# Kernel optimization log

Hardware: AMD Instinct MI355X
Metric: run time of the kernel (lower is better)

## Reference

```python
import jax, jax.numpy as jnp
import numpy as np

B, T, C = 4, 2048, 2048
H, N = 32, 64  # heads, head_size
EPS = 1e-5


def setup_inputs() -> dict:
    key = jax.random.key(0)
    ks = jax.random.split(key, 16)
    s = 0.02
    return {
        'hidden': jax.random.normal(ks[0], (B, T, C), jnp.float32),
        'time_decay': jax.random.normal(ks[1], (H, N), jnp.float32),
        'time_first': jax.random.normal(ks[2], (H, N), jnp.float32),
        'Wr': jax.random.normal(ks[3], (C, C), jnp.float32) * s,
        'Wk': jax.random.normal(ks[4], (C, C), jnp.float32) * s,
        'Wv': jax.random.normal(ks[5], (C, C), jnp.float32) * s,
        'Wg': jax.random.normal(ks[6], (C, C), jnp.float32) * s,
        'Wo': jax.random.normal(ks[7], (C, C), jnp.float32) * s,
        'mix_r': jax.random.uniform(ks[8], (1, 1, C), jnp.float32),
        'mix_k': jax.random.uniform(ks[9], (1, 1, C), jnp.float32),
        'mix_v': jax.random.uniform(ks[10], (1, 1, C), jnp.float32),
        'mix_g': jax.random.uniform(ks[11], (1, 1, C), jnp.float32),
        'ln_w': jax.random.uniform(ks[12], (C,), jnp.float32, 0.5, 1.5),
        'ln_b': jax.random.normal(ks[13], (C,), jnp.float32) * 0.1,
        'init_state': jnp.zeros((B, H, N, N), jnp.float32),
    }


def reference(hidden, time_decay, time_first, Wr, Wk, Wv, Wg, Wo,
              mix_r, mix_k, mix_v, mix_g, ln_w, ln_b, init_state):
    b, t, c = hidden.shape
    h, n = time_decay.shape
    # time shift: shifted[:, 0] = 0 (fresh state), shifted[:, i] = hidden[:, i-1]
    shifted = jnp.pad(hidden, ((0, 0), (1, 0), (0, 0)))[:, :-1]
    xk = hidden * mix_k + shifted * (1.0 - mix_k)
    xv = hidden * mix_v + shifted * (1.0 - mix_v)
    xr = hidden * mix_r + shifted * (1.0 - mix_r)
    xg = hidden * mix_g + shifted * (1.0 - mix_g)

    r = (xr @ Wr).astype(jnp.float32).reshape(b, t, h, n)
    k = (xk @ Wk).astype(jnp.float32).reshape(b, t, h, n)
    v = (xv @ Wv).astype(jnp.float32).reshape(b, t, h, n)
    gate = jax.nn.silu(xg @ Wg)  # [b,t,c]

    w = jnp.exp(-jnp.exp(time_decay.astype(jnp.float32)))  # [h,n] decay per k-channel
    u = time_first.astype(jnp.float32)                      # [h,n]

    def step(state, rkv):
        rt, kt, vt = rkv  # each [b,h,n]
        at = kt[..., :, None] * vt[..., None, :]  # outer product kt @ vt -> [b,h,n,n]
        out_t = jnp.einsum('bhn,bhnm->bhm', rt, u[None, :, :, None] * at + state)
        new_state = at + w[None, :, :, None] * state
        return new_state, out_t

    rT = jnp.moveaxis(r, 1, 0)  # [t,b,h,n]
    kT = jnp.moveaxis(k, 1, 0)
    vT = jnp.moveaxis(v, 1, 0)
    final_state, outT = jax.lax.scan(step, init_state.astype(jnp.float32), (rT, kT, vT))
    out = jnp.moveaxis(outT, 0, 1)  # [b,t,h,n]

    # GroupNorm with num_groups = h over the c = h*n channels
    mean = out.mean(-1, keepdims=True)
    var = out.var(-1, keepdims=True)
    out = (out - mean) / jnp.sqrt(var + EPS)
    out = out.reshape(b, t, c) * ln_w + ln_b

    out = out.astype(hidden.dtype) * gate
    out = out @ Wo
    return out, final_state
```

## Files before the change

### kernel.cpp

```cpp
#include <hip/hip_runtime.h>
#include <stdint.h>

typedef unsigned short ushort_t;
typedef __attribute__((ext_vector_type(8))) short bf16x8;
typedef __attribute__((ext_vector_type(4))) float f32x4;
typedef __attribute__((ext_vector_type(8))) unsigned short u16x8;

__device__ __forceinline__ ushort_t f2bf(float f) {
  union { float f; unsigned u; } v; v.f = f;
  unsigned r = v.u + 0x7fffu + ((v.u >> 16) & 1u);
  return (ushort_t)(r >> 16);
}
__device__ __forceinline__ float bf2f(ushort_t u) {
  union { unsigned u; float f; } v; v.u = ((unsigned)u) << 16;
  return v.f;
}

__device__ __forceinline__ void gload_lds16(const void* g, void* l) {
  __builtin_amdgcn_global_load_lds(
      (const __attribute__((address_space(1))) void*)g,
      (__attribute__((address_space(3))) void*)l, 16, 0, 0);
}

struct PrepArgs {
  const float* W[5];
  ushort_t* Wt[5];
  const float* Hd;
  const float* mr; const float* mk; const float* mv; const float* mg;
  ushort_t* xr; ushort_t* xk; ushort_t* xv; ushort_t* xg;
};

__global__ __launch_bounds__(256) void prep(PrepArgs a, int n, int Mrows, int Tt) {
  const int z = blockIdx.z;
  if (z < 5) {
    const float* __restrict__ W = a.W[z];
    ushort_t* __restrict__ Wt = a.Wt[z];
    __shared__ float tile[32][33];
    const int tx = threadIdx.x & 31, ty = threadIdx.x >> 5;
    const int bx = blockIdx.x, by = blockIdx.y;
#pragma unroll
    for (int r = 0; r < 4; ++r)
      tile[ty + 8 * r][tx] = W[(size_t)(by * 32 + ty + 8 * r) * n + bx * 32 + tx];
    __syncthreads();
#pragma unroll
    for (int r = 0; r < 4; ++r)
      Wt[(size_t)(bx * 32 + ty + 8 * r) * n + by * 32 + tx] =
          f2bf(tile[tx][ty + 8 * r]);
    return;
  }
  const int Cc = n;
  const float* __restrict__ Hd = a.Hd;
  const size_t n8 = (size_t)Mrows * Cc / 8;
  const int bid = blockIdx.y * gridDim.x + blockIdx.x;
  for (size_t idx = (size_t)bid * blockDim.x + threadIdx.x; idx < n8;
       idx += (size_t)gridDim.x * gridDim.y * blockDim.x) {
    const size_t e = idx * 8;
    const int m = (int)(e / (size_t)Cc);
    const int c = (int)(e % (size_t)Cc);
    const int t = m % Tt;
    f32x4 h0 = *(const f32x4*)&Hd[e];
    f32x4 h1 = *(const f32x4*)&Hd[e + 4];
    f32x4 sA = {0.f, 0.f, 0.f, 0.f}, sB = {0.f, 0.f, 0.f, 0.f};
    if (t != 0) {
      sA = *(const f32x4*)&Hd[e - Cc];
      sB = *(const f32x4*)&Hd[e - Cc + 4];
    }
    f32x4 mA[4], mB[4];
    mA[0] = *(const f32x4*)&a.mr[c]; mB[0] = *(const f32x4*)&a.mr[c + 4];
    mA[1] = *(const f32x4*)&a.mk[c]; mB[1] = *(const f32x4*)&a.mk[c + 4];
    mA[2] = *(const f32x4*)&a.mv[c]; mB[2] = *(const f32x4*)&a.mv[c + 4];
    mA[3] = *(const f32x4*)&a.mg[c]; mB[3] = *(const f32x4*)&a.mg[c + 4];
    u16x8 o[4];
#pragma unroll
    for (int w = 0; w < 4; ++w) {
#pragma unroll
      for (int q = 0; q < 4; ++q) {
        o[w][q]     = f2bf(sA[q] + (h0[q] - sA[q]) * mA[w][q]);
        o[w][q + 4] = f2bf(sB[q] + (h1[q] - sB[q]) * mB[w][q]);
      }
    }
    *(u16x8*)&a.xr[e] = o[0];
    *(u16x8*)&a.xk[e] = o[1];
    *(u16x8*)&a.xv[e] = o[2];
    *(u16x8*)&a.xg[e] = o[3];
  }
}

struct GemmArgs {
  const ushort_t* A[4];
  const ushort_t* Bt[4];
  void* C[4];
};

__device__ __forceinline__ void stage_mat(const ushort_t* __restrict__ base,
                                          int K, int voff, char* ldsmat,
                                          int tid) {
#pragma unroll
  for (int hf = 0; hf < 2; ++hf)
#pragma unroll
    for (int s = 0; s < 2; ++s)
      gload_lds16(base + (size_t)(hf * 128 + s * 64) * K + voff,
                  ldsmat + hf * 16384 + s * 8192 + tid * 16);
}

template <int BF16OUT>
__global__ __launch_bounds__(512, 1) void gemm256(GemmArgs args, int M, int N, int K) {
  extern __shared__ char lds[];
  const int z = blockIdx.z;
  const ushort_t* __restrict__ A = args.A[z];
  const ushort_t* __restrict__ Bt = args.Bt[z];

  const int tid = threadIdx.x;
  const int lane = tid & 63, w = tid >> 6;
  const int wm = w >> 2, wn = w & 3;
  const int r16 = lane & 15, kb = lane >> 4;

  const int nbx = N >> 8;
  const int nwg = nbx * (M >> 8);
  const int orig = blockIdx.y * nbx + blockIdx.x;
  const int wid = (orig & 7) * (nwg >> 3) + (orig >> 3);
  const int bm0 = (wid / nbx) << 8;
  const int bn0 = (wid % nbx) << 8;

  const int trow = tid >> 3;
  const int voff = trow * K + (((((tid & 7) * 16) ^ ((trow & 7) << 4))) >> 1);
  const ushort_t* __restrict__ Abase = A + (size_t)bm0 * K;
  const ushort_t* __restrict__ Bbase = Bt + (size_t)bn0 * K;

  int aoff[8], boff[4];
#pragma unroll
  for (int mi = 0; mi < 8; ++mi) {
    const int d = (mi * 16 + r16) * 128 + kb * 16;
    aoff[mi] = wm * 16384 + (d ^ (((d >> 7) & 7) << 4));
  }
#pragma unroll
  for (int ni = 0; ni < 4; ++ni) {
    const int d = ((wn & 1) * 64 + ni * 16 + r16) * 128 + kb * 16;
    boff[ni] = 32768 + (wn >> 1) * 16384 + (d ^ (((d >> 7) & 7) << 4));
  }

  f32x4 acc[8][4] = {};
  const int NT = K >> 6;

  stage_mat(Abase, K, voff, lds, tid);
  stage_mat(Bbase, K, voff, lds + 32768, tid);
  stage_mat(Abase + 64, K, voff, lds + 65536, tid);
  stage_mat(Bbase + 64, K, voff, lds + 65536 + 32768, tid);
  asm volatile("s_waitcnt vmcnt(8)" ::: "memory");
  asm volatile("s_barrier" ::: "memory");

  for (int t = 0; t < NT; ++t) {
    const int cur = t & 1;
    char* cbase = lds + cur * 65536;
    bf16x8 ah[4][2], bq[4][2];

#pragma unroll
    for (int m = 0; m < 4; ++m) {
      ah[m][0] = *(const bf16x8*)(cbase + aoff[m]);
      ah[m][1] = *(const bf16x8*)(cbase + (aoff[m] ^ 64));
    }
#pragma unroll
    for (int n = 0; n < 2; ++n) {
      bq[n][0] = *(const bf16x8*)(cbase + boff[n]);
      bq[n][1] = *(const bf16x8*)(cbase + (boff[n] ^ 64));
    }
    asm volatile("s_barrier" ::: "memory");
    __builtin_amdgcn_s_setprio(1);
#pragma unroll
    for (int m = 0; m < 4; ++m)
#pragma unroll
      for (int n = 0; n < 2; ++n)
#pragma unroll
        for (int ks = 0; ks < 2; ++ks)
          acc[m][n] = __builtin_amdgcn_mfma_f32_16x16x32_bf16(
              ah[m][ks], bq[n][ks], acc[m][n], 0, 0, 0);
    __builtin_amdgcn_s_setprio(0);

#pragma unroll
    for (int n = 2; n < 4; ++n) {
      bq[n][0] = *(const bf16x8*)(cbase + boff[n]);
      bq[n][1] = *(const bf16x8*)(cbase + (boff[n] ^ 64));
    }
    asm volatile("s_barrier" ::: "memory");
    __builtin_amdgcn_s_setprio(1);
#pragma unroll
    for (int m = 0; m < 4; ++m)
#pragma unroll
      for (int n = 2; n < 4; ++n)
#pragma unroll
        for (int ks = 0; ks < 2; ++ks)
          acc[m][n] = __builtin_amdgcn_mfma_f32_16x16x32_bf16(
              ah[m][ks], bq[n][ks], acc[m][n], 0, 0, 0);
    __builtin_amdgcn_s_setprio(0);

#pragma unroll
    for (int m = 0; m < 4; ++m) {
      ah[m][0] = *(const bf16x8*)(cbase + aoff[4 + m]);
      ah[m][1] = *(const bf16x8*)(cbase + (aoff[4 + m] ^ 64));
    }
    asm volatile("s_barrier" ::: "memory");
    if (t + 2 < NT)
      stage_mat(Abase + (t + 2) * 64, K, voff, cbase, tid);
    __builtin_amdgcn_s_setprio(1);
#pragma unroll
    for (int m = 0; m < 4; ++m)
#pragma unroll
      for (int n = 0; n < 2; ++n)
#pragma unroll
        for (int ks = 0; ks < 2; ++ks)
          acc[4 + m][n] = __builtin_amdgcn_mfma_f32_16x16x32_bf16(
              ah[m][ks], bq[n][ks], acc[4 + m][n], 0, 0, 0);

    if (t + 2 < NT)
      stage_mat(Bbase + (t + 2) * 64, K, voff, cbase + 32768, tid);
#pragma unroll
    for (int m = 0; m < 4; ++m)
#pragma unroll
      for (int n = 2; n < 4; ++n)
#pragma unroll
        for (int ks = 0; ks < 2; ++ks)
          acc[4 + m][n] = __builtin_amdgcn_mfma_f32_16x16x32_bf16(
              ah[m][ks], bq[n][ks], acc[4 + m][n], 0, 0, 0);
    __builtin_amdgcn_s_setprio(0);

    if (t + 1 < NT) {
      if (t + 2 < NT)
        asm volatile("s_waitcnt vmcnt(8)" ::: "memory");
      else
        asm volatile("s_waitcnt vmcnt(0)" ::: "memory");
      asm volatile("s_barrier" ::: "memory");
    }
  }

  const int row0 = bm0 + wm * 128 + kb * 4;
  const int col0 = bn0 + wn * 64 + r16;
#pragma unroll
  for (int mi = 0; mi < 8; ++mi)
#pragma unroll
    for (int ni = 0; ni < 4; ++ni) {
      f32x4 v = acc[mi][ni];
      const int row = row0 + mi * 16;
      const int col = col0 + ni * 16;
#pragma unroll
      for (int rr = 0; rr < 4; ++rr) {
        if (BF16OUT)
          ((ushort_t*)args.C[z])[(size_t)(row + rr) * N + col] = f2bf(v[rr]);
        else
          ((float*)args.C[z])[(size_t)(row + rr) * N + col] = v[rr];
      }
    }
}

__global__ __launch_bounds__(512, 1) void wkv_chunk(
    const ushort_t* __restrict__ Rm, const ushort_t* __restrict__ Km,
    const ushort_t* __restrict__ Vm, const float* __restrict__ td,
    const float* __restrict__ tf,
    float* __restrict__ Oatt, float* __restrict__ chunkA,
    int Tt, int Hh, int NC, int Lc) {
  extern __shared__ char smem[];
  ushort_t* Rs = (ushort_t*)(smem + 0);
  ushort_t* Ks = (ushort_t*)(smem + 18432);
  ushort_t* Vt = (ushort_t*)(smem + 36864);
  ushort_t* Kt = (ushort_t*)(smem + 54272);
  ushort_t* At = (ushort_t*)(smem + 71680);
  float* wp  = (float*)(smem + 106496);
  float* u_  = (float*)(smem + 110848);
  float* l2w = (float*)(smem + 111104);

  const int blk = blockIdx.x;
  const int bh = blk / NC, c = blk % NC;
  const int b = bh / Hh, h = bh % Hh;
  const int tid = threadIdx.x;
  const int lane = tid & 63, w = tid >> 6;
  const int r16 = lane & 15, g = lane >> 4;
  const int Cc = Hh * 64;
  const size_t base = ((size_t)b * Tt + (size_t)c * Lc) * Cc + h * 64;

  {
    const int srow = tid >> 2;
    const int scol = (tid & 3) * 16;
    const size_t gb = base + (size_t)srow * Cc + scol;
    u16x8 r0 = *(const u16x8*)&Rm[gb];
    u16x8 r1 = *(const u16x8*)&Rm[gb + 8];
    u16x8 k0 = *(const u16x8*)&Km[gb];
    u16x8 k1 = *(const u16x8*)&Km[gb + 8];
    u16x8 v0 = *(const u16x8*)&Vm[gb];
    u16x8 v1 = *(const u16x8*)&Vm[gb + 8];
    *(u16x8*)&Rs[srow * 72 + scol] = r0;
    *(u16x8*)&Rs[srow * 72 + scol + 8] = r1;
    *(u16x8*)&Ks[srow * 72 + scol] = k0;
    *(u16x8*)&Ks[srow * 72 + scol + 8] = k1;
#pragma unroll
    for (int e = 0; e < 8; ++e) {
      Kt[(scol + e) * 136 + srow] = k0[e];
      Kt[(scol + 8 + e) * 136 + srow] = k1[e];
      Vt[(scol + e) * 136 + srow] = v0[e];
      Vt[(scol + 8 + e) * 136 + srow] = v1[e];
    }
    if (tid < 64) {
      const float ev = expf(td[h * 64 + tid]);
      const float wv = expf(-ev);
      u_[tid] = tf[h * 64 + tid];
      l2w[tid] = -1.44269504f * ev;
      float p = 1.f;
#pragma unroll
      for (int d = 0; d < 16; ++d) { wp[d * 68 + tid] = p; p *= wv; }
    }
    const u16x8 z = {};
    for (int o = tid; o < (128 * 136) / 8; o += 512) *(u16x8*)&At[o * 8] = z;
  }
  __syncthreads();

  for (int p = w; p < 28; p += 8) {
    int tau = 1, cum = 0;
    while (cum + tau <= p) { cum += tau; ++tau; }
    const int sig = p - cum;
    const float dd = (float)((tau - sig) * 16 - 1 - r16);
    f32x4 acc = {0.f, 0.f, 0.f, 0.f};
#pragma unroll
    for (int ks = 0; ks < 2; ++ks) {
      const int ib = ks * 32 + g * 8;
      u16x8 rv = *(const u16x8*)&Rs[(tau * 16 + r16) * 72 + ib];
      u16x8 kv = *(const u16x8*)&Ks[(sig * 16 + r16) * 72 + ib];
      f32x4 wa = *(const f32x4*)&wp[r16 * 68 + ib];
      f32x4 wb = *(const f32x4*)&wp[r16 * 68 + ib + 4];
      f32x4 la = *(const f32x4*)&l2w[ib];
      f32x4 lb = *(const f32x4*)&l2w[ib + 4];
      union { bf16x8 v; ushort_t s[8]; } af, bfr;
#pragma unroll
      for (int e = 0; e < 4; ++e) {
        af.s[e]     = f2bf(bf2f(rv[e]) * wa[e]);
        af.s[e + 4] = f2bf(bf2f(rv[e + 4]) * wb[e]);
        bfr.s[e]     = f2bf(bf2f(kv[e]) * exp2f(dd * la[e]));
        bfr.s[e + 4] = f2bf(bf2f(kv[e + 4]) * exp2f(dd * lb[e]));
      }
      acc = __builtin_amdgcn_mfma_f32_16x16x32_bf16(af.v, bfr.v, acc, 0, 0, 0);
    }
#pragma unroll
    for (int r = 0; r < 4; ++r)
      At[(tau * 16 + g * 4 + r) * 136 + sig * 16 + r16] = f2bf(acc[r]);
  }

  for (int rr = 0; rr < 3; ++rr) {
    const int eid = tid + rr * 512;
    if (eid >= 1088) break;
    const int tile = eid / 136;
    const int e2 = eid % 136;
    int t = 0, cum = 0;
    while (cum + t + 1 <= e2) { cum += t + 1; ++t; }
    const int s = e2 - cum;
    const ushort_t* rrow = &Rs[(tile * 16 + t) * 72];
    const ushort_t* krow = &Ks[(tile * 16 + s) * 72];
    const float* frow = (s < t) ? &wp[(t - s - 1) * 68] : u_;
    float acc = 0.f;
#pragma unroll
    for (int i0 = 0; i0 < 64; i0 += 8) {
      u16x8 rv = *(const u16x8*)&rrow[i0];
      u16x8 kv = *(const u16x8*)&krow[i0];
      f32x4 f0 = *(const f32x4*)&frow[i0];
      f32x4 f1 = *(const f32x4*)&frow[i0 + 4];
#pragma unroll
      for (int e = 0; e < 4; ++e) {
        acc = fmaf(bf2f(rv[e]), bf2f(kv[e]) * f0[e], acc);
        acc = fmaf(bf2f(rv[e + 4]), bf2f(kv[e + 4]) * f1[e], acc);
      }
    }
    At[(tile * 16 + t) * 136 + tile * 16 + s] = f2bf(acc);
  }
  __syncthreads();

  {
    const int nk = (w + 2) >> 1;
#pragma unroll
    for (int jt = 0; jt < 4; ++jt) {
      f32x4 acc = {0.f, 0.f, 0.f, 0.f};
      for (int kk = 0; kk < nk; ++kk) {
        bf16x8 af = *(const bf16x8*)&At[(w * 16 + r16) * 136 + kk * 32 + g * 8];
        bf16x8 bv = *(const bf16x8*)&Vt[(jt * 16 + r16) * 136 + kk * 32 + g * 8];
        acc = __builtin_amdgcn_mfma_f32_16x16x32_bf16(af, bv, acc, 0, 0, 0);
      }
#pragma unroll
      for (int r = 0; r < 4; ++r)
        Oatt[base + (size_t)(w * 16 + g * 4 + r) * Cc + jt * 16 + r16] = acc[r];
    }
  }

#pragma unroll
  for (int q = 0; q < 2; ++q) {
    const int T = w * 2 + q;
    const int it = T >> 2, jt = T & 3;
    const float li = l2w[it * 16 + r16];
    f32x4 acc = {0.f, 0.f, 0.f, 0.f};
#pragma unroll
    for (int kk = 0; kk < 4; ++kk) {
      const int s0 = kk * 32 + g * 8;
      u16x8 kr = *(const u16x8*)&Kt[(it * 16 + r16) * 136 + s0];
      bf16x8 bv = *(const bf16x8*)&Vt[(jt * 16 + r16) * 136 + s0];
      union { bf16x8 v; ushort_t s[8]; } af;
#pragma unroll
      for (int e = 0; e < 8; ++e)
        af.s[e] = f2bf(bf2f(kr[e]) * exp2f((float)(127 - (s0 + e)) * li));
      acc = __builtin_amdgcn_mfma_f32_16x16x32_bf16(af.v, bv, acc, 0, 0, 0);
    }
#pragma unroll
    for (int r = 0; r < 4; ++r)
      chunkA[(size_t)blk * 4096 + (it * 16 + g * 4 + r) * 64 + jt * 16 + r16] =
          acc[r];
  }
}

__global__ __launch_bounds__(256) void chunk_carry(
    const float* __restrict__ chunkA, const float* __restrict__ s0,
    const float* __restrict__ td,
    float* __restrict__ chunkS, float* __restrict__ Sout,
    int Hh, int NC, int Lc) {
  const int blk = blockIdx.x;
  const int bh = blk >> 2, q = blk & 3;
  const int h = bh % Hh;
  const int e4 = q * 1024 + threadIdx.x * 4;
  const int i = e4 >> 6;
  const float wL = expf(-(float)Lc * expf(td[h * 64 + i]));
  f32x4 S = *(const f32x4*)&s0[(size_t)bh * 4096 + e4];
  for (int c = 0; c < NC; ++c) {
    *(f32x4*)&chunkS[((size_t)bh * NC + c) * 4096 + e4] = S;
    f32x4 A = *(const f32x4*)&chunkA[((size_t)bh * NC + c) * 4096 + e4];
#pragma unroll
    for (int t = 0; t < 4; ++t) S[t] = fmaf(wL, S[t], A[t]);
  }
  *(f32x4*)&Sout[(size_t)bh * 4096 + e4] = S;
}

__global__ __launch_bounds__(256) void chunk_out(
    const float* __restrict__ OattIn, const float* __restrict__ chunkS,
    const ushort_t* __restrict__ Rm, const ushort_t* __restrict__ Gm,
    const float* __restrict__ td,
    const float* __restrict__ lnw, const float* __restrict__ lnb,
    ushort_t* __restrict__ Xo, int Tt, int Hh, int NC, int Lc) {
  __shared__ float rL[128 * 64];
  const int blk = blockIdx.x;
  const int bh = blk / NC, c = blk % NC;
  const int b = bh / Hh, h = bh % Hh;
  const int tid = threadIdx.x;
  const int Cc = Hh * 64;
  const size_t rowbase = (size_t)b * Tt + (size_t)c * Lc;

  {
    const int i0 = (tid & 7) * 8;
    const int tb = tid >> 3;
    float e8[8];
#pragma unroll
    for (int qq = 0; qq < 8; ++qq) e8[qq] = expf(td[h * 64 + i0 + qq]);
#pragma unroll
    for (int m = 0; m < 4; ++m) {
      const int tau = tb + 32 * m;
      u16x8 rv = *(const u16x8*)&Rm[(rowbase + tau) * Cc + h * 64 + i0];
#pragma unroll
      for (int qq = 0; qq < 8; ++qq)
        rL[tau * 64 + i0 + qq] = bf2f(rv[qq]) * expf(-(float)tau * e8[qq]);
    }
  }

  const int lane = tid & 63, wv = tid >> 6;
  float Sc[64];
  {
    const float* Sp = chunkS + (size_t)blk * 4096 + lane;
#pragma unroll
    for (int i = 0; i < 64; ++i) Sc[i] = Sp[i * 64];
  }
  const float lw = lnw[h * 64 + lane];
  const float lb = lnb[h * 64 + lane];
  __syncthreads();

  for (int k = 0; k < Lc / 4; ++k) {
    const int tau = wv + 4 * k;
    const size_t goff = (rowbase + tau) * Cc + h * 64 + lane;
    float ac0 = OattIn[goff], ac1 = 0.f;
#pragma unroll
    for (int i0 = 0; i0 < 64; i0 += 8) {
      f32x4 rv0 = *(const f32x4*)&rL[tau * 64 + i0];
      f32x4 rv1 = *(const f32x4*)&rL[tau * 64 + i0 + 4];
      ac0 = fmaf(rv0[0], Sc[i0], ac0);
      ac0 = fmaf(rv0[1], Sc[i0 + 1], ac0);
      ac0 = fmaf(rv0[2], Sc[i0 + 2], ac0);
      ac0 = fmaf(rv0[3], Sc[i0 + 3], ac0);
      ac1 = fmaf(rv1[0], Sc[i0 + 4], ac1);
      ac1 = fmaf(rv1[1], Sc[i0 + 5], ac1);
      ac1 = fmaf(rv1[2], Sc[i0 + 6], ac1);
      ac1 = fmaf(rv1[3], Sc[i0 + 7], ac1);
    }
    const float acc = ac0 + ac1;
    float s = acc, s2 = acc * acc;
#pragma unroll
    for (int m = 1; m < 64; m <<= 1) {
      s += __shfl_xor(s, m);
      s2 += __shfl_xor(s2, m);
    }
    const float mean = s * (1.f / 64.f);
    const float var = s2 * (1.f / 64.f) - mean * mean;
    const float inv = 1.f / sqrtf(var + 1e-5f);
    const float y = (acc - mean) * inv * lw + lb;
    const float gv = bf2f(Gm[goff]);
    const float gate = gv / (1.f + expf(-gv));
    Xo[goff] = f2bf(y * gate);
  }
}

extern "C" void kernel_launch(void* const* d_in, const int* in_sizes, int n_in,
                              void* d_out, int out_size, void* d_ws, size_t ws_size,
                              hipStream_t stream) {
  const int B = 4, T = 2048, Cc = 2048, H = 32;
  const int M = B * T;
  const int NC = 16, Lc = 128;

  const float* hidden = (const float*)d_in[0];
  const float* td     = (const float*)d_in[1];
  const float* tf     = (const float*)d_in[2];
  const float* Wr     = (const float*)d_in[3];
  const float* Wk     = (const float*)d_in[4];
  const float* Wv     = (const float*)d_in[5];
  const float* Wg     = (const float*)d_in[6];
  const float* Wo     = (const float*)d_in[7];
  const float* mix_r  = (const float*)d_in[8];
  const float* mix_k  = (const float*)d_in[9];
  const float* mix_v  = (const float*)d_in[10];
  const float* mix_g  = (const float*)d_in[11];
  const float* lnw    = (const float*)d_in[12];
  const float* lnb    = (const float*)d_in[13];
  const float* s0     = (const float*)d_in[14];

  const size_t SZ_WT = (size_t)Cc * Cc * 2;
  const size_t SZ_X  = (size_t)M * Cc * 2;
  const size_t NEED  = 5 * SZ_WT + 6 * SZ_X;

  if (ws_size < NEED) return;

  float* out  = (float*)d_out;
  float* sfin = (float*)d_out + (size_t)M * Cc;
  ushort_t* xg = (ushort_t*)d_out;
  ushort_t* gb = (ushort_t*)d_out + (size_t)M * Cc;

  char* ws = (char*)d_ws;
  ushort_t* wt[5];
  for (int z = 0; z < 5; ++z) wt[z] = (ushort_t*)(ws + z * SZ_WT);
  char* regX = ws + 5 * SZ_WT;
  char* regY = regX + 3 * SZ_X;
  ushort_t* xr = (ushort_t*)regX;
  ushort_t* xk = (ushort_t*)(regX + SZ_X);
  ushort_t* xv = (ushort_t*)(regX + 2 * SZ_X);
  ushort_t* rb = (ushort_t*)regY;
  ushort_t* kb = (ushort_t*)(regY + SZ_X);
  ushort_t* vb = (ushort_t*)(regY + 2 * SZ_X);
  float* oatt   = (float*)regX;
  float* chunkA = (float*)(regX + 2 * SZ_X);
  float* chunkS = (float*)(regY + SZ_X);
  ushort_t* xo  = (ushort_t*)(regY + 2 * SZ_X);

  {
    PrepArgs a;
    a.W[0] = Wr; a.W[1] = Wk; a.W[2] = Wv; a.W[3] = Wg; a.W[4] = Wo;
    for (int z = 0; z < 5; ++z) a.Wt[z] = wt[z];
    a.Hd = hidden;
    a.mr = mix_r; a.mk = mix_k; a.mv = mix_v; a.mg = mix_g;
    a.xr = xr; a.xk = xk; a.xv = xv; a.xg = xg;
    dim3 g(Cc / 32, Cc / 32, 6);
    prep<<<g, 256, 0, stream>>>(a, Cc, M, T);
  }

  {
    GemmArgs a;
    a.A[0] = xr; a.A[1] = xk; a.A[2] = xv; a.A[3] = xg;
    for (int z = 0; z < 4; ++z) a.Bt[z] = wt[z];
    a.C[0] = rb; a.C[1] = kb; a.C[2] = vb; a.C[3] = gb;
    dim3 g(Cc / 256, M / 256, 4);
    gemm256<1><<<g, 512, 131072, stream>>>(a, M, Cc, Cc);
  }

  wkv_chunk<<<B * H * NC, 512, 111616, stream>>>(rb, kb, vb, td, tf, oatt,
                                                 chunkA, T, H, NC, Lc);
  chunk_carry<<<B * H * 4, 256, 0, stream>>>(chunkA, s0, td, chunkS, sfin,
                                             H, NC, Lc);
  chunk_out<<<B * H * NC, 256, 0, stream>>>(oatt, chunkS, rb, gb, td, lnw, lnb,
                                            xo, T, H, NC, Lc);

  {
    GemmArgs a = {};
    a.A[0] = xo; a.Bt[0] = wt[4]; a.C[0] = out;
    dim3 g(Cc / 256, M / 256, 1);
    gemm256<0><<<g, 512, 131072, stream>>>(a, M, Cc, Cc);
  }
}
```

Before: 585.5 us.

## Precompute decay-scaled K tiles in LDS and split projection GEMM launches

In the chunked WKV kernel, K is pre-scaled once by decay powers (a w^j table plus a w^16q table) and stored in a new LDS buffer Ks2 and in the transposed Kt. This removes the per-element exp2f calls from the inter-tile attention loop and from the chunk-state loop, and the R side now uses a product of two table entries. LDS use rises to about 131 KB. The four projection GEMMs are also split from one batched z=4 launch into four separate launches, which adds launch overhead and serialization. Rebuilding the decay factor as a product of two powers can change rounding slightly.

```diff
diff --git a/kernel.cpp b/kernel.cpp
--- a/kernel.cpp
+++ b/kernel.cpp
@@ -258,14 +258,15 @@
     float* __restrict__ Oatt, float* __restrict__ chunkA,
     int Tt, int Hh, int NC, int Lc) {
   extern __shared__ char smem[];
-  ushort_t* Rs = (ushort_t*)(smem + 0);
-  ushort_t* Ks = (ushort_t*)(smem + 18432);
-  ushort_t* Vt = (ushort_t*)(smem + 36864);
-  ushort_t* Kt = (ushort_t*)(smem + 54272);
-  ushort_t* At = (ushort_t*)(smem + 71680);
-  float* wp  = (float*)(smem + 106496);
-  float* u_  = (float*)(smem + 110848);
-  float* l2w = (float*)(smem + 111104);
+  ushort_t* Rs  = (ushort_t*)(smem + 0);
+  ushort_t* Ks  = (ushort_t*)(smem + 18432);
+  ushort_t* Ks2 = (ushort_t*)(smem + 36864);
+  ushort_t* Vt  = (ushort_t*)(smem + 55296);
+  ushort_t* Kt  = (ushort_t*)(smem + 72704);
+  ushort_t* At  = (ushort_t*)(smem + 90112);
+  float* wp   = (float*)(smem + 124928);
+  float* w16p = (float*)(smem + 129280);
+  float* u_   = (float*)(smem + 131456);
 
   const int blk = blockIdx.x;
   const int bh = blk / NC, c = blk % NC;
@@ -276,35 +277,52 @@
   const int Cc = Hh * 64;
   const size_t base = ((size_t)b * Tt + (size_t)c * Lc) * Cc + h * 64;
 
+  const int srow = tid >> 2;
+  const int scol = (tid & 3) * 16;
+  const size_t gb = base + (size_t)srow * Cc + scol;
+  u16x8 r0 = *(const u16x8*)&Rm[gb];
+  u16x8 r1 = *(const u16x8*)&Rm[gb + 8];
+  u16x8 k0 = *(const u16x8*)&Km[gb];
+  u16x8 k1 = *(const u16x8*)&Km[gb + 8];
+  u16x8 v0 = *(const u16x8*)&Vm[gb];
+  u16x8 v1 = *(const u16x8*)&Vm[gb + 8];
+
+  if (tid < 64) {
+    const float ev = expf(td[h * 64 + tid]);
+    const float wv = expf(-ev);
+    u_[tid] = tf[h * 64 + tid];
+    float p = 1.f;
+#pragma unroll
+    for (int d = 0; d < 16; ++d) { wp[d * 68 + tid] = p; p *= wv; }
+    float pq = 1.f;
+#pragma unroll
+    for (int q = 0; q < 8; ++q) { w16p[q * 68 + tid] = pq; pq *= p; }
+  }
+  __syncthreads();
+
   {
-    const int srow = tid >> 2;
-    const int scol = (tid & 3) * 16;
-    const size_t gb = base + (size_t)srow * Cc + scol;
-    u16x8 r0 = *(const u16x8*)&Rm[gb];
-    u16x8 r1 = *(const u16x8*)&Rm[gb + 8];
-    u16x8 k0 = *(const u16x8*)&Km[gb];
-    u16x8 k1 = *(const u16x8*)&Km[gb + 8];
-    u16x8 v0 = *(const u16x8*)&Vm[gb];
-    u16x8 v1 = *(const u16x8*)&Vm[gb + 8];
     *(u16x8*)&Rs[srow * 72 + scol] = r0;
     *(u16x8*)&Rs[srow * 72 + scol + 8] = r1;
     *(u16x8*)&Ks[srow * 72 + scol] = k0;
     *(u16x8*)&Ks[srow * 72 + scol + 8] = k1;
+    const int s16 = srow & 15, shi = srow >> 4;
+    const float* fa = &wp[(15 - s16) * 68 + scol];
+    const float* gq = &w16p[(7 - shi) * 68 + scol];
+    u16x8 a2, b2;
 #pragma unroll
     for (int e = 0; e < 8; ++e) {
-      Kt[(scol + e) * 136 + srow] = k0[e];
-      Kt[(scol + 8 + e) * 136 + srow] = k1[e];
+      a2[e] = f2bf(bf2f(k0[e]) * fa[e]);
+      b2[e] = f2bf(bf2f(k1[e]) * fa[e + 8]);
+    }
+    *(u16x8*)&Ks2[srow * 72 + scol] = a2;
+    *(u16x8*)&Ks2[srow * 72 + scol + 8] = b2;
+#pragma unroll
+    for (int e = 0; e < 8; ++e) {
       Vt[(scol + e) * 136 + srow] = v0[e];
       Vt[(scol + 8 + e) * 136 + srow] = v1[e];
-    }
-    if (tid < 64) {
-      const float ev = expf(td[h * 64 + tid]);
-      const float wv = expf(-ev);
-      u_[tid] = tf[h * 64 + tid];
-      l2w[tid] = -1.44269504f * ev;
-      float p = 1.f;
-#pragma unroll
-      for (int d = 0; d < 16; ++d) { wp[d * 68 + tid] = p; p *= wv; }
+      Kt[(scol + e) * 136 + srow] = f2bf(bf2f(k0[e]) * fa[e] * gq[e]);
+      Kt[(scol + 8 + e) * 136 + srow] =
+          f2bf(bf2f(k1[e]) * fa[e + 8] * gq[e + 8]);
     }
     const u16x8 z = {};
     for (int o = tid; o < (128 * 136) / 8; o += 512) *(u16x8*)&At[o * 8] = z;
@@ -315,26 +333,25 @@
     int tau = 1, cum = 0;
     while (cum + tau <= p) { cum += tau; ++tau; }
     const int sig = p - cum;
-    const float dd = (float)((tau - sig) * 16 - 1 - r16);
+    const float* wr  = &wp[r16 * 68];
+    const float* w16 = &w16p[(tau - sig - 1) * 68];
     f32x4 acc = {0.f, 0.f, 0.f, 0.f};
 #pragma unroll
     for (int ks = 0; ks < 2; ++ks) {
       const int ib = ks * 32 + g * 8;
       u16x8 rv = *(const u16x8*)&Rs[(tau * 16 + r16) * 72 + ib];
-      u16x8 kv = *(const u16x8*)&Ks[(sig * 16 + r16) * 72 + ib];
-      f32x4 wa = *(const f32x4*)&wp[r16 * 68 + ib];
-      f32x4 wb = *(const f32x4*)&wp[r16 * 68 + ib + 4];
-      f32x4 la = *(const f32x4*)&l2w[ib];
-      f32x4 lb = *(const f32x4*)&l2w[ib + 4];
-      union { bf16x8 v; ushort_t s[8]; } af, bfr;
+      bf16x8 kv = *(const bf16x8*)&Ks2[(sig * 16 + r16) * 72 + ib];
+      f32x4 wa = *(const f32x4*)&wr[ib];
+      f32x4 wb = *(const f32x4*)&wr[ib + 4];
+      f32x4 sa = *(const f32x4*)&w16[ib];
+      f32x4 sb = *(const f32x4*)&w16[ib + 4];
+      union { bf16x8 v; ushort_t s[8]; } af;
 #pragma unroll
       for (int e = 0; e < 4; ++e) {
-        af.s[e]     = f2bf(bf2f(rv[e]) * wa[e]);
-        af.s[e + 4] = f2bf(bf2f(rv[e + 4]) * wb[e]);
-        bfr.s[e]     = f2bf(bf2f(kv[e]) * exp2f(dd * la[e]));
-        bfr.s[e + 4] = f2bf(bf2f(kv[e + 4]) * exp2f(dd * lb[e]));
+        af.s[e]     = f2bf(bf2f(rv[e]) * (wa[e] * sa[e]));
+        af.s[e + 4] = f2bf(bf2f(rv[e + 4]) * (wb[e] * sb[e]));
       }
-      acc = __builtin_amdgcn_mfma_f32_16x16x32_bf16(af.v, bfr.v, acc, 0, 0, 0);
+      acc = __builtin_amdgcn_mfma_f32_16x16x32_bf16(af.v, kv, acc, 0, 0, 0);
     }
 #pragma unroll
     for (int r = 0; r < 4; ++r)
@@ -389,18 +406,13 @@
   for (int q = 0; q < 2; ++q) {
     const int T = w * 2 + q;
     const int it = T >> 2, jt = T & 3;
-    const float li = l2w[it * 16 + r16];
     f32x4 acc = {0.f, 0.f, 0.f, 0.f};
 #pragma unroll
     for (int kk = 0; kk < 4; ++kk) {
       const int s0 = kk * 32 + g * 8;
-      u16x8 kr = *(const u16x8*)&Kt[(it * 16 + r16) * 136 + s0];
+      bf16x8 af = *(const bf16x8*)&Kt[(it * 16 + r16) * 136 + s0];
       bf16x8 bv = *(const bf16x8*)&Vt[(jt * 16 + r16) * 136 + s0];
-      union { bf16x8 v; ushort_t s[8]; } af;
-#pragma unroll
-      for (int e = 0; e < 8; ++e)
-        af.s[e] = f2bf(bf2f(kr[e]) * exp2f((float)(127 - (s0 + e)) * li));
-      acc = __builtin_amdgcn_mfma_f32_16x16x32_bf16(af.v, bv, acc, 0, 0, 0);
+      acc = __builtin_amdgcn_mfma_f32_16x16x32_bf16(af, bv, acc, 0, 0, 0);
     }
 #pragma unroll
     for (int r = 0; r < 4; ++r)
@@ -567,15 +579,17 @@
   }
 
   {
-    GemmArgs a;
-    a.A[0] = xr; a.A[1] = xk; a.A[2] = xv; a.A[3] = xg;
-    for (int z = 0; z < 4; ++z) a.Bt[z] = wt[z];
-    a.C[0] = rb; a.C[1] = kb; a.C[2] = vb; a.C[3] = gb;
-    dim3 g(Cc / 256, M / 256, 4);
-    gemm256<1><<<g, 512, 131072, stream>>>(a, M, Cc, Cc);
-  }
-
-  wkv_chunk<<<B * H * NC, 512, 111616, stream>>>(rb, kb, vb, td, tf, oatt,
+    const ushort_t* As[4] = {xr, xk, xv, xg};
+    void* Cs[4] = {rb, kb, vb, gb};
+    for (int z = 0; z < 4; ++z) {
+      GemmArgs a = {};
+      a.A[0] = As[z]; a.Bt[0] = wt[z]; a.C[0] = Cs[z];
+      dim3 g(Cc / 256, M / 256, 1);
+      gemm256<1><<<g, 512, 131072, stream>>>(a, M, Cc, Cc);
+    }
+  }
+
+  wkv_chunk<<<B * H * NC, 512, 131712, stream>>>(rb, kb, vb, td, tf, oatt,
                                                  chunkA, T, H, NC, Lc);
   chunk_carry<<<B * H * 4, 256, 0, stream>>>(chunkA, s0, td, chunkS, sfin,
                                              H, NC, Lc);
```

Measured after the change: 585.2 us. Within noise of the previous version (-0.0%).
